# Optimization experiments

Measured on AMD Instinct MI355X. Metric: run time of the kernel, lower is better.

Reference implementation:

```python
import jax, jax.numpy as jnp
import numpy as np

N = 100000      # nodes
E = 1600000     # edges
F_IN = 512      # num_features
H = 128         # hidden
C = 40          # num_classes
K = 10          # Chebyshev order


def setup_inputs() -> dict:
    key = jax.random.key(0)
    ks = jax.random.split(key, 6)
    x = jax.random.normal(ks[0], (N, F_IN), dtype=jnp.float32)
    edge_index = jax.random.randint(ks[1], (2, E), 0, N, dtype=jnp.int32)
    W1 = jax.random.normal(ks[2], (F_IN, H), dtype=jnp.float32) / np.sqrt(F_IN).astype(np.float32)
    b1 = jnp.zeros((H,), dtype=jnp.float32)
    W2 = jax.random.normal(ks[3], (H, C), dtype=jnp.float32) / np.sqrt(H).astype(np.float32)
    b2 = jnp.zeros((C,), dtype=jnp.float32)
    # Chebyshev coefficients temp[K+1]
    temp = 1.0 + 0.1 * jax.random.normal(ks[4], (K + 1,), dtype=jnp.float32)
    return {"x": x, "edge_index": edge_index, "W1": W1, "b1": b1, "W2": W2, "b2": b2, "temp": temp}


def reference(x, edge_index, W1, b1, W2, b2, temp):
    # MLP encoder (eval mode: dropout is identity)
    h = jax.nn.relu(x @ W1 + b1)          # [N, H]
    h = h @ W2 + b2                        # [N, C]

    # gcn_norm: add self-loops, symmetric normalization
    self_loop = jnp.arange(N, dtype=edge_index.dtype)
    row = jnp.concatenate([edge_index[0], self_loop])   # [E+N]
    col = jnp.concatenate([edge_index[1], self_loop])
    deg = jax.ops.segment_sum(jnp.ones_like(row, dtype=jnp.float32), row, num_segments=N)
    dis = jnp.where(deg > 0, jax.lax.rsqrt(jnp.maximum(deg, 1.0)), 0.0)
    norm = dis[row] * dis[col]             # [E+N]

    def prop(v):  # A_hat @ v : gather-scale-scatter over edges
        return jax.ops.segment_sum(norm[:, None] * v[col], row, num_segments=N)

    # Chebyshev recurrence: Tx_k = 2*A_hat*Tx_{k-1} - Tx_{k-2}
    Tx0 = h
    Tx1 = prop(h)
    out0 = temp[0] * Tx0 + temp[1] * Tx1

    def body(carry, coe):
        t0, t1, acc = carry
        t2 = 2.0 * prop(t1) - t0
        return (t1, t2, acc + coe * t2), None

    (_, _, out), _ = jax.lax.scan(body, (Tx0, Tx1, out0), temp[2:])
    return jax.nn.log_softmax(out, axis=1)
```

## Files before the change

### kernel.cpp

```cpp
#include <hip/hip_runtime.h>
#include <hip/hip_bf16.h>
#include <cstdint>
#include <cstddef>

#define NN   100000
#define EE   1600000
#define FIN  512
#define HID  128
#define CC   40
#define KORD 10

typedef __attribute__((ext_vector_type(4))) float f4;
typedef __attribute__((ext_vector_type(8))) short short8_t;
typedef __attribute__((ext_vector_type(2))) unsigned int u2;

__device__ __forceinline__ unsigned short cvt_bf16(float f) {
  union { float f; unsigned u; } a; a.f = f;
  unsigned r = a.u + 0x7fffu + ((a.u >> 16) & 1u);
  return (unsigned short)(r >> 16);
}
__device__ __forceinline__ unsigned pk_bf(float a, float b) {
  union { float f; unsigned u; } x, y; x.f = a; y.f = b;
  unsigned ra = x.u + 0x7fffu + ((x.u >> 16) & 1u);
  unsigned rb = y.u + 0x7fffu + ((y.u >> 16) & 1u);
  return (ra >> 16) | (rb & 0xffff0000u);
}
__device__ __forceinline__ f4 cvf(u2 p) {
  union { unsigned u; float f; } a, b, c, d;
  a.u = p.x << 16; b.u = p.x & 0xffff0000u;
  c.u = p.y << 16; d.u = p.y & 0xffff0000u;
  f4 r; r.x = a.f; r.y = b.f; r.z = c.f; r.w = d.f; return r;
}

__global__ __launch_bounds__(256) void k_deg(const int* __restrict__ rowI, int* __restrict__ deg) {
  int i = blockIdx.x * 256 + threadIdx.x;
  if (i < EE) atomicAdd(&deg[rowI[i]], 1);
}

__global__ __launch_bounds__(256) void k_finalize(int* __restrict__ deg, float* __restrict__ dis,
                                                  float* __restrict__ sqd, float* __restrict__ invd) {
  int i = blockIdx.x * 256 + threadIdx.x;
  if (i < NN) {
    int d = deg[i] + 1;
    deg[i] = d;
    float fd = (float)d;
    dis[i]  = rsqrtf(fd);
    sqd[i]  = sqrtf(fd);
    invd[i] = 1.0f / fd;
  }
}

__global__ __launch_bounds__(256) void k_scan1(const int* __restrict__ cnt, int* __restrict__ excl,
                                               int* __restrict__ bsums) {
  __shared__ int s[256];
  int tid = threadIdx.x;
  int base = blockIdx.x * 1024 + tid * 4;
  int v0 = (base + 0 < NN) ? cnt[base + 0] : 0;
  int v1 = (base + 1 < NN) ? cnt[base + 1] : 0;
  int v2 = (base + 2 < NN) ? cnt[base + 2] : 0;
  int v3 = (base + 3 < NN) ? cnt[base + 3] : 0;
  int tsum = v0 + v1 + v2 + v3;
  s[tid] = tsum;
  __syncthreads();
  for (int off = 1; off < 256; off <<= 1) {
    int t = (tid >= off) ? s[tid - off] : 0;
    __syncthreads();
    if (tid >= off) s[tid] += t;
    __syncthreads();
  }
  int run = s[tid] - tsum;
  if (tid == 255) bsums[blockIdx.x] = s[255];
  if (base + 0 < NN) excl[base + 0] = run; run += v0;
  if (base + 1 < NN) excl[base + 1] = run; run += v1;
  if (base + 2 < NN) excl[base + 2] = run; run += v2;
  if (base + 3 < NN) excl[base + 3] = run;
}

__global__ __launch_bounds__(128) void k_scan2(int* __restrict__ bsums, int nb) {
  __shared__ int s[128];
  int tid = threadIdx.x;
  int v = (tid < nb) ? bsums[tid] : 0;
  s[tid] = v;
  __syncthreads();
  for (int off = 1; off < 128; off <<= 1) {
    int t = (tid >= off) ? s[tid - off] : 0;
    __syncthreads();
    if (tid >= off) s[tid] += t;
    __syncthreads();
  }
  if (tid < nb) bsums[tid] = s[tid] - v;
}

__global__ __launch_bounds__(256) void k_scan3(const int* __restrict__ cnt, int* __restrict__ rs,
                                               int* __restrict__ cur, const int* __restrict__ bsums) {
  int i = blockIdx.x * 256 + threadIdx.x;
  if (i < NN) {
    int v = rs[i] + bsums[i >> 10];
    rs[i] = v;
    cur[i] = v;
    if (i == NN - 1) rs[NN] = v + cnt[i];
  }
}

__global__ __launch_bounds__(256) void k_scatter(const int* __restrict__ rowI, const int* __restrict__ colI,
                                                 int* __restrict__ cur, int* __restrict__ colS) {
  int i = blockIdx.x * 256 + threadIdx.x;
  if (i >= EE + NN) return;
  int r, c;
  if (i < EE) { r = rowI[i]; c = colI[i]; }
  else        { r = i - EE;  c = r; }
  int pos = atomicAdd(&cur[r], 1);
  colS[pos] = c * 80;
}

__global__ __launch_bounds__(256) void k_w1t(const float* __restrict__ W1, unsigned short* __restrict__ W1T) {
  int idx = blockIdx.x * 256 + threadIdx.x;
  int k = idx >> 7;
  int n = idx & 127;
  float v = W1[idx];
  W1T[(k >> 5) * 4096 + n * 32 + (k & 31)] = cvt_bf16(v);
}

#define LDK 40
__global__ __launch_bounds__(256) void k_gemm1(const float* __restrict__ x, const unsigned short* __restrict__ W1T,
                                               const float* __restrict__ b1, float* __restrict__ h1) {
  __shared__ __align__(16) short As_s[128][LDK];
  __shared__ __align__(16) short Bs_s[128][LDK];
  int tid  = threadIdx.x;
  int wave = tid >> 6, lane = tid & 63;
  int blockRow = blockIdx.x * 128;
  int wr = (wave & 1) * 64, wc = (wave >> 1) * 64;
  int l15 = lane & 15, lk = (lane >> 4) * 8;

  int ar = tid >> 1, ak = (tid & 1) * 16;

  f4 acc[4][4] = {};

  for (int k0 = 0; k0 < FIN; k0 += 32) {
    int gr = blockRow + ar;
    f4 xv0 = {0.f,0.f,0.f,0.f}, xv1 = xv0, xv2 = xv0, xv3 = xv0;
    if (gr < NN) {
      const float* xr = x + (size_t)gr * FIN + k0 + ak;
      xv0 = *(const f4*)&xr[0];
      xv1 = *(const f4*)&xr[4];
      xv2 = *(const f4*)&xr[8];
      xv3 = *(const f4*)&xr[12];
    }
    short8_t p0, p1;
#pragma unroll
    for (int q = 0; q < 4; ++q) {
      p0[q]     = (short)cvt_bf16(xv0[q]);
      p0[q + 4] = (short)cvt_bf16(xv1[q]);
      p1[q]     = (short)cvt_bf16(xv2[q]);
      p1[q + 4] = (short)cvt_bf16(xv3[q]);
    }
    *(short8_t*)&As_s[ar][ak]     = p0;
    *(short8_t*)&As_s[ar][ak + 8] = p1;

    const unsigned short* Wt = W1T + (k0 >> 5) * 4096;
    short8_t q0 = *(const short8_t*)&Wt[tid * 16];
    short8_t q1 = *(const short8_t*)&Wt[tid * 16 + 8];
    int bn = tid >> 1, bkk = (tid & 1) * 16;
    *(short8_t*)&Bs_s[bn][bkk]     = q0;
    *(short8_t*)&Bs_s[bn][bkk + 8] = q1;

    __syncthreads();

    short8_t afr[4], bfr[4];
#pragma unroll
    for (int m = 0; m < 4; ++m) afr[m] = *(const short8_t*)&As_s[wr + m * 16 + l15][lk];
#pragma unroll
    for (int n = 0; n < 4; ++n) bfr[n] = *(const short8_t*)&Bs_s[wc + n * 16 + l15][lk];
#pragma unroll
    for (int m = 0; m < 4; ++m)
#pragma unroll
      for (int n = 0; n < 4; ++n)
        acc[m][n] = __builtin_amdgcn_mfma_f32_16x16x32_bf16(afr[m], bfr[n], acc[m][n], 0, 0, 0);

    __syncthreads();
  }

  float bias[4];
#pragma unroll
  for (int n = 0; n < 4; ++n) bias[n] = b1[wc + n * 16 + l15];
#pragma unroll
  for (int m = 0; m < 4; ++m) {
    int baseRow = blockRow + wr + m * 16 + (lane >> 4) * 4;
#pragma unroll
    for (int n = 0; n < 4; ++n) {
      int col = wc + n * 16 + l15;
#pragma unroll
      for (int r = 0; r < 4; ++r) {
        int grow = baseRow + r;
        if (grow < NN) h1[(size_t)grow * HID + col] = fmaxf(acc[m][n][r] + bias[n], 0.f);
      }
    }
  }
}

__global__ __launch_bounds__(256) void k_gemm2(const float* __restrict__ h1, const float* __restrict__ W2,
                                               const float* __restrict__ b2, const float* __restrict__ temp,
                                               const float* __restrict__ dis,
                                               float* __restrict__ w0, float* __restrict__ outAcc) {
  __shared__ float sW[HID * CC];
  __shared__ float sb[CC];
  int tid = threadIdx.x;
  for (int i = tid; i < HID * CC; i += 256) sW[i] = W2[i];
  if (tid < CC) sb[tid] = b2[tid];
  __syncthreads();
  int gid = blockIdx.x * 256 + tid;
  int row = gid / CC;
  int col = gid - row * CC;
  const float* hr = h1 + (size_t)row * HID;
  float acc = sb[col];
#pragma unroll 8
  for (int k = 0; k < HID; ++k) acc = fmaf(hr[k], sW[k * CC + col], acc);
  outAcc[gid] = temp[0] * acc;
  w0[gid] = acc * dis[row];
}

__global__ __launch_bounds__(256) void k_cvt(const float* __restrict__ v, unsigned short* __restrict__ sh) {
  int i = blockIdx.x * 256 + threadIdx.x;
  if (i * 4 >= NN * CC) return;
  f4 t = *(const f4*)&v[i * 4];
  u2 p; p.x = pk_bf(t.x, t.y); p.y = pk_bf(t.z, t.w);
  *(u2*)&sh[i * 4] = p;
}

template <int MODE>
__global__ __launch_bounds__(256) void k_prop(const unsigned short* __restrict__ shIn,
                                              unsigned short* __restrict__ shOut,
                                              float* __restrict__ vio,
                                              float* __restrict__ outAcc,
                                              const int* __restrict__ colS,
                                              const int* __restrict__ rs,
                                              const float* __restrict__ invd, const float* __restrict__ sqd,
                                              const float* __restrict__ temp, int kIdx) {
  int lane = threadIdx.x & 63;
  int wave = threadIdx.x >> 6;
  int sub  = lane / 10;
  int fi   = lane - sub * 10;
  int node = blockIdx.x * 24 + wave * 6 + sub;
  bool active = (sub < 6) && (node < NN);
  int s = 0, e = 0;
  if (active) { s = rs[node]; e = rs[node + 1]; }
  const char* base = (const char*)shIn + fi * 8;
  f4 a0 = {0.f,0.f,0.f,0.f}, a1 = a0, a2 = a0, a3 = a0;
  int j = s;
  for (; j + 8 <= e; j += 8) {
    int c0 = colS[j],     c1 = colS[j + 1], c2 = colS[j + 2], c3 = colS[j + 3];
    int c4 = colS[j + 4], c5 = colS[j + 5], c6 = colS[j + 6], c7 = colS[j + 7];
    u2 p0 = *(const u2*)(base + c0);
    u2 p1 = *(const u2*)(base + c1);
    u2 p2 = *(const u2*)(base + c2);
    u2 p3 = *(const u2*)(base + c3);
    u2 p4 = *(const u2*)(base + c4);
    u2 p5 = *(const u2*)(base + c5);
    u2 p6 = *(const u2*)(base + c6);
    u2 p7 = *(const u2*)(base + c7);
    a0 += cvf(p0); a1 += cvf(p1); a2 += cvf(p2); a3 += cvf(p3);
    a0 += cvf(p4); a1 += cvf(p5); a2 += cvf(p6); a3 += cvf(p7);
  }
  if (j + 4 <= e) {
    int c0 = colS[j], c1 = colS[j + 1], c2 = colS[j + 2], c3 = colS[j + 3];
    u2 p0 = *(const u2*)(base + c0);
    u2 p1 = *(const u2*)(base + c1);
    u2 p2 = *(const u2*)(base + c2);
    u2 p3 = *(const u2*)(base + c3);
    a0 += cvf(p0); a1 += cvf(p1); a2 += cvf(p2); a3 += cvf(p3);
    j += 4;
  }
  if (j + 2 <= e) {
    u2 p0 = *(const u2*)(base + colS[j]);
    u2 p1 = *(const u2*)(base + colS[j + 1]);
    a0 += cvf(p0); a1 += cvf(p1);
    j += 2;
  }
  if (j < e) a2 += cvf(*(const u2*)(base + colS[j]));

  if (active) {
    f4 sum = (a0 + a1) + (a2 + a3);
    float iv = invd[node], sq = sqd[node], tk = temp[kIdx];
    size_t o = (size_t)node * CC + fi * 4;
    f4 w;
    if (MODE == 0) w = iv * sum;
    else { f4 prev = *(const f4*)&vio[o]; w = (2.f * iv) * sum - prev; }
    *(f4*)&vio[o] = w;
    u2 p; p.x = pk_bf(w.x, w.y); p.y = pk_bf(w.z, w.w);
    *(u2*)((char*)shOut + (size_t)node * 80 + fi * 8) = p;
    f4 oa = *(const f4*)&outAcc[o];
    *(f4*)&outAcc[o] = oa + (tk * sq) * w;
  }
}

__global__ __launch_bounds__(256) void k_lsm(float* __restrict__ out) {
  int row = blockIdx.x * 256 + threadIdx.x;
  if (row >= NN) return;
  float* p = out + (size_t)row * CC;
  float v[CC];
#pragma unroll
  for (int i = 0; i < CC / 4; ++i) *(f4*)&v[i * 4] = *(const f4*)&p[i * 4];
  float m = v[0];
#pragma unroll
  for (int i = 1; i < CC; ++i) m = fmaxf(m, v[i]);
  float ssum = 0.f;
#pragma unroll
  for (int i = 0; i < CC; ++i) ssum += expf(v[i] - m);
  float lse = m + logf(ssum);
#pragma unroll
  for (int i = 0; i < CC; ++i) v[i] -= lse;
#pragma unroll
  for (int i = 0; i < CC / 4; ++i) *(f4*)&p[i * 4] = *(f4*)&v[i * 4];
}

extern "C" void kernel_launch(void* const* d_in, const int* in_sizes, int n_in,
                              void* d_out, int out_size, void* d_ws, size_t ws_size,
                              hipStream_t stream) {
  const float* x    = (const float*)d_in[0];
  const int*   ei   = (const int*)d_in[1];
  const float* W1   = (const float*)d_in[2];
  const float* b1   = (const float*)d_in[3];
  const float* W2   = (const float*)d_in[4];
  const float* b2   = (const float*)d_in[5];
  const float* temp = (const float*)d_in[6];
  const int* rowI = ei;
  const int* colI = ei + EE;
  float* out = (float*)d_out;

  char* w = (char*)d_ws;
  auto alloc = [&](size_t bytes) -> void* {
    void* p = (void*)w;
    w += (bytes + 255) & ~(size_t)255;
    return p;
  };
  float* t0    = (float*)alloc((size_t)NN * CC * 4);
  float* t1    = (float*)alloc((size_t)NN * CC * 4);
  int*   deg   = (int*)  alloc((size_t)NN * 4);
  float* dis   = (float*)alloc((size_t)NN * 4);
  float* sqd   = (float*)alloc((size_t)NN * 4);
  float* invd  = (float*)alloc((size_t)NN * 4);
  int*   rs    = (int*)  alloc((size_t)(NN + 1) * 4);
  int*   cur   = (int*)  alloc((size_t)NN * 4);
  int*   bsums = (int*)  alloc(512 * 4);
  unsigned short* W1T = (unsigned short*)alloc((size_t)FIN * HID * 2);
  char* big = (char*)alloc((size_t)NN * HID * 4);
  float* h1 = (float*)big;
  int*   colS = (int*)big;
  unsigned short* sh0 = (unsigned short*)(big + ((size_t)8 << 20));
  unsigned short* sh1 = (unsigned short*)(big + ((size_t)16 << 20));

  hipMemsetAsync(deg, 0, (size_t)NN * 4, stream);

  k_deg<<<(EE + 255) / 256, 256, 0, stream>>>(rowI, deg);
  k_finalize<<<(NN + 255) / 256, 256, 0, stream>>>(deg, dis, sqd, invd);

  int nb = (NN + 1023) / 1024;
  k_scan1<<<nb, 256, 0, stream>>>(deg, rs, bsums);
  k_scan2<<<1, 128, 0, stream>>>(bsums, nb);
  k_scan3<<<(NN + 255) / 256, 256, 0, stream>>>(deg, rs, cur, bsums);

  k_w1t<<<FIN * HID / 256, 256, 0, stream>>>(W1, W1T);
  k_gemm1<<<(NN + 127) / 128, 256, 0, stream>>>(x, W1T, b1, h1);
  k_gemm2<<<(NN * CC) / 256, 256, 0, stream>>>(h1, W2, b2, temp, dis, t0, out);

  k_scatter<<<(EE + NN + 255) / 256, 256, 0, stream>>>(rowI, colI, cur, colS);
  k_cvt<<<(NN * CC / 4 + 255) / 256, 256, 0, stream>>>(t0, sh0);

  int G = (NN + 23) / 24;
  unsigned short* sh[2] = {sh0, sh1};
  float* tb[2] = {t0, t1};
  k_prop<0><<<G, 256, 0, stream>>>(sh[0], sh[1], t1, out, colS, rs, invd, sqd, temp, 1);
  for (int k = 2; k <= KORD; ++k) {
    k_prop<1><<<G, 256, 0, stream>>>(sh[(k - 1) & 1], sh[k & 1], tb[k & 1], out, colS, rs, invd, sqd, temp, k);
  }

  k_lsm<<<(NN + 255) / 256, 256, 0, stream>>>(out);
}
```

Baseline: 745.5 us.

## Fuse setup kernels, degree-sort nodes, widen prop gathers to 16 bytes

Several small setup kernels are merged into combined launches: degree counting with the W1 transpose, scan2 with a histogram scan, scan3 with building a degree-sorted permutation, and the edge scatter with the GEMM1 launch. The scatter now runs alongside GEMM1 instead of after it, which requires colS to move to its own buffer rather than aliasing h1. The propagation kernel now assigns 5 lanes per node with 16-byte bf16 gathers, 12 nodes per wave, and processes nodes in degree-sorted order for better load balance. This reduces launch count and per-edge load instructions, at the cost of extra atomics and a permutation indirection that breaks sequential output writes.

```diff
diff --git a/kernel.cpp b/kernel.cpp
--- a/kernel.cpp
+++ b/kernel.cpp
@@ -12,7 +12,7 @@
 
 typedef __attribute__((ext_vector_type(4))) float f4;
 typedef __attribute__((ext_vector_type(8))) short short8_t;
-typedef __attribute__((ext_vector_type(2))) unsigned int u2;
+typedef __attribute__((ext_vector_type(4))) unsigned int u4;
 
 __device__ __forceinline__ unsigned short cvt_bf16(float f) {
   union { float f; unsigned u; } a; a.f = f;
@@ -25,20 +25,30 @@
   unsigned rb = y.u + 0x7fffu + ((y.u >> 16) & 1u);
   return (ra >> 16) | (rb & 0xffff0000u);
 }
-__device__ __forceinline__ f4 cvf(u2 p) {
+__device__ __forceinline__ f4 cvf2(unsigned lo, unsigned hi) {
   union { unsigned u; float f; } a, b, c, d;
-  a.u = p.x << 16; b.u = p.x & 0xffff0000u;
-  c.u = p.y << 16; d.u = p.y & 0xffff0000u;
+  a.u = lo << 16; b.u = lo & 0xffff0000u;
+  c.u = hi << 16; d.u = hi & 0xffff0000u;
   f4 r; r.x = a.f; r.y = b.f; r.z = c.f; r.w = d.f; return r;
 }
 
-__global__ __launch_bounds__(256) void k_deg(const int* __restrict__ rowI, int* __restrict__ deg) {
-  int i = blockIdx.x * 256 + threadIdx.x;
-  if (i < EE) atomicAdd(&deg[rowI[i]], 1);
+__global__ __launch_bounds__(256) void k_dw(const int* __restrict__ rowI, int* __restrict__ deg,
+                                            const float* __restrict__ W1, unsigned short* __restrict__ W1T,
+                                            int ndeg) {
+  int b = blockIdx.x;
+  if (b < ndeg) {
+    int i = b * 256 + threadIdx.x;
+    if (i < EE) atomicAdd(&deg[rowI[i]], 1);
+  } else {
+    int idx = (b - ndeg) * 256 + threadIdx.x;
+    int k = idx >> 7, n = idx & 127;
+    W1T[(k >> 5) * 4096 + n * 32 + (k & 31)] = cvt_bf16(W1[idx]);
+  }
 }
 
 __global__ __launch_bounds__(256) void k_finalize(int* __restrict__ deg, float* __restrict__ dis,
-                                                  float* __restrict__ sqd, float* __restrict__ invd) {
+                                                  float* __restrict__ sqd, float* __restrict__ invd,
+                                                  int* __restrict__ hist) {
   int i = blockIdx.x * 256 + threadIdx.x;
   if (i < NN) {
     int d = deg[i] + 1;
@@ -47,6 +57,7 @@
     dis[i]  = rsqrtf(fd);
     sqd[i]  = sqrtf(fd);
     invd[i] = 1.0f / fd;
+    atomicAdd(&hist[min(d, 255)], 1);
   }
 }
 
@@ -76,62 +87,85 @@
   if (base + 3 < NN) excl[base + 3] = run;
 }
 
-__global__ __launch_bounds__(128) void k_scan2(int* __restrict__ bsums, int nb) {
-  __shared__ int s[128];
+__global__ __launch_bounds__(256) void k_scan2h(int* __restrict__ bsums, int nb, int* __restrict__ hist) {
+  __shared__ int s[256];
   int tid = threadIdx.x;
-  int v = (tid < nb) ? bsums[tid] : 0;
-  s[tid] = v;
-  __syncthreads();
-  for (int off = 1; off < 128; off <<= 1) {
-    int t = (tid >= off) ? s[tid - off] : 0;
-    __syncthreads();
-    if (tid >= off) s[tid] += t;
-    __syncthreads();
-  }
-  if (tid < nb) bsums[tid] = s[tid] - v;
-}
-
-__global__ __launch_bounds__(256) void k_scan3(const int* __restrict__ cnt, int* __restrict__ rs,
-                                               int* __restrict__ cur, const int* __restrict__ bsums) {
-  int i = blockIdx.x * 256 + threadIdx.x;
-  if (i < NN) {
-    int v = rs[i] + bsums[i >> 10];
-    rs[i] = v;
-    cur[i] = v;
-    if (i == NN - 1) rs[NN] = v + cnt[i];
-  }
-}
-
-__global__ __launch_bounds__(256) void k_scatter(const int* __restrict__ rowI, const int* __restrict__ colI,
-                                                 int* __restrict__ cur, int* __restrict__ colS) {
-  int i = blockIdx.x * 256 + threadIdx.x;
-  if (i >= EE + NN) return;
-  int r, c;
-  if (i < EE) { r = rowI[i]; c = colI[i]; }
-  else        { r = i - EE;  c = r; }
-  int pos = atomicAdd(&cur[r], 1);
-  colS[pos] = c * 80;
-}
-
-__global__ __launch_bounds__(256) void k_w1t(const float* __restrict__ W1, unsigned short* __restrict__ W1T) {
-  int idx = blockIdx.x * 256 + threadIdx.x;
-  int k = idx >> 7;
-  int n = idx & 127;
-  float v = W1[idx];
-  W1T[(k >> 5) * 4096 + n * 32 + (k & 31)] = cvt_bf16(v);
+  if (blockIdx.x == 0) {
+    int v = (tid < nb) ? bsums[tid] : 0;
+    s[tid] = v;
+    __syncthreads();
+    for (int off = 1; off < 256; off <<= 1) {
+      int t = (tid >= off) ? s[tid - off] : 0;
+      __syncthreads();
+      if (tid >= off) s[tid] += t;
+      __syncthreads();
+    }
+    if (tid < nb) bsums[tid] = s[tid] - v;
+  } else {
+    int v = hist[tid];
+    s[tid] = v;
+    __syncthreads();
+    for (int off = 1; off < 256; off <<= 1) {
+      int t = (tid >= off) ? s[tid - off] : 0;
+      __syncthreads();
+      if (tid >= off) s[tid] += t;
+      __syncthreads();
+    }
+    hist[tid] = s[tid] - v;
+  }
+}
+
+__global__ __launch_bounds__(256) void k_scan3p(const int* __restrict__ cnt, int* __restrict__ rs,
+                                                int* __restrict__ cur, const int* __restrict__ bsums,
+                                                const int* __restrict__ hoff, int* __restrict__ hcnt,
+                                                int* __restrict__ perm, int nb3) {
+  int b = blockIdx.x;
+  int tid = threadIdx.x;
+  if (b < nb3) {
+    int i = b * 256 + tid;
+    if (i < NN) {
+      int v = rs[i] + bsums[i >> 10];
+      rs[i] = v;
+      cur[i] = v;
+      if (i == NN - 1) rs[NN] = v + cnt[i];
+    }
+  } else {
+    int i = (b - nb3) * 256 + tid;
+    if (i < NN) {
+      int d = min(cnt[i], 255);
+      int pos = hoff[d] + atomicAdd(&hcnt[d], 1);
+      perm[pos] = i;
+    }
+  }
 }
 
 #define LDK 40
-__global__ __launch_bounds__(256) void k_gemm1(const float* __restrict__ x, const unsigned short* __restrict__ W1T,
-                                               const float* __restrict__ b1, float* __restrict__ h1) {
+__global__ __launch_bounds__(256) void k_g1sc(const float* __restrict__ x, const unsigned short* __restrict__ W1T,
+                                              const float* __restrict__ b1, float* __restrict__ h1,
+                                              const int* __restrict__ rowI, const int* __restrict__ colI,
+                                              int* __restrict__ cur, int* __restrict__ colS, int ng1) {
   __shared__ __align__(16) short As_s[128][LDK];
   __shared__ __align__(16) short Bs_s[128][LDK];
+  if (blockIdx.x >= ng1) {
+    int bid = blockIdx.x - ng1;
+#pragma unroll
+    for (int t = 0; t < 4; ++t) {
+      int i = bid * 1024 + t * 256 + threadIdx.x;
+      if (i < EE + NN) {
+        int r, c;
+        if (i < EE) { r = rowI[i]; c = colI[i]; }
+        else        { r = i - EE;  c = r; }
+        int pos = atomicAdd(&cur[r], 1);
+        colS[pos] = c * 80;
+      }
+    }
+    return;
+  }
   int tid  = threadIdx.x;
   int wave = tid >> 6, lane = tid & 63;
   int blockRow = blockIdx.x * 128;
   int wr = (wave & 1) * 64, wc = (wave >> 1) * 64;
   int l15 = lane & 15, lk = (lane >> 4) * 8;
-
   int ar = tid >> 1, ak = (tid & 1) * 16;
 
   f4 acc[4][4] = {};
@@ -223,8 +257,9 @@
   int i = blockIdx.x * 256 + threadIdx.x;
   if (i * 4 >= NN * CC) return;
   f4 t = *(const f4*)&v[i * 4];
-  u2 p; p.x = pk_bf(t.x, t.y); p.y = pk_bf(t.z, t.w);
-  *(u2*)&sh[i * 4] = p;
+  unsigned lo = pk_bf(t.x, t.y), hi = pk_bf(t.z, t.w);
+  unsigned long long p = (unsigned long long)lo | ((unsigned long long)hi << 32);
+  *(unsigned long long*)&sh[i * 4] = p;
 }
 
 template <int MODE>
@@ -234,62 +269,69 @@
                                               float* __restrict__ outAcc,
                                               const int* __restrict__ colS,
                                               const int* __restrict__ rs,
+                                              const int* __restrict__ perm,
                                               const float* __restrict__ invd, const float* __restrict__ sqd,
                                               const float* __restrict__ temp, int kIdx) {
   int lane = threadIdx.x & 63;
   int wave = threadIdx.x >> 6;
-  int sub  = lane / 10;
-  int fi   = lane - sub * 10;
-  int node = blockIdx.x * 24 + wave * 6 + sub;
-  bool active = (sub < 6) && (node < NN);
-  int s = 0, e = 0;
-  if (active) { s = rs[node]; e = rs[node + 1]; }
-  const char* base = (const char*)shIn + fi * 8;
-  f4 a0 = {0.f,0.f,0.f,0.f}, a1 = a0, a2 = a0, a3 = a0;
+  int grp  = lane / 5;
+  int fi   = lane - grp * 5;
+  int nidx = blockIdx.x * 48 + wave * 12 + grp;
+  bool active = (grp < 12) && (nidx < NN);
+  int node = 0, s = 0, e = 0;
+  if (active) { node = perm[nidx]; s = rs[node]; e = rs[node + 1]; }
+  const char* base = (const char*)shIn + fi * 16;
+  f4 lo0 = {0.f,0.f,0.f,0.f}, hi0 = lo0, lo1 = lo0, hi1 = lo0;
+  f4 lo2 = lo0, hi2 = lo0, lo3 = lo0, hi3 = lo0;
   int j = s;
-  for (; j + 8 <= e; j += 8) {
-    int c0 = colS[j],     c1 = colS[j + 1], c2 = colS[j + 2], c3 = colS[j + 3];
-    int c4 = colS[j + 4], c5 = colS[j + 5], c6 = colS[j + 6], c7 = colS[j + 7];
-    u2 p0 = *(const u2*)(base + c0);
-    u2 p1 = *(const u2*)(base + c1);
-    u2 p2 = *(const u2*)(base + c2);
-    u2 p3 = *(const u2*)(base + c3);
-    u2 p4 = *(const u2*)(base + c4);
-    u2 p5 = *(const u2*)(base + c5);
-    u2 p6 = *(const u2*)(base + c6);
-    u2 p7 = *(const u2*)(base + c7);
-    a0 += cvf(p0); a1 += cvf(p1); a2 += cvf(p2); a3 += cvf(p3);
-    a0 += cvf(p4); a1 += cvf(p5); a2 += cvf(p6); a3 += cvf(p7);
-  }
-  if (j + 4 <= e) {
+  for (; j + 4 <= e; j += 4) {
     int c0 = colS[j], c1 = colS[j + 1], c2 = colS[j + 2], c3 = colS[j + 3];
-    u2 p0 = *(const u2*)(base + c0);
-    u2 p1 = *(const u2*)(base + c1);
-    u2 p2 = *(const u2*)(base + c2);
-    u2 p3 = *(const u2*)(base + c3);
-    a0 += cvf(p0); a1 += cvf(p1); a2 += cvf(p2); a3 += cvf(p3);
-    j += 4;
+    u4 p0 = *(const u4*)(base + c0);
+    u4 p1 = *(const u4*)(base + c1);
+    u4 p2 = *(const u4*)(base + c2);
+    u4 p3 = *(const u4*)(base + c3);
+    lo0 += cvf2(p0.x, p0.y); hi0 += cvf2(p0.z, p0.w);
+    lo1 += cvf2(p1.x, p1.y); hi1 += cvf2(p1.z, p1.w);
+    lo2 += cvf2(p2.x, p2.y); hi2 += cvf2(p2.z, p2.w);
+    lo3 += cvf2(p3.x, p3.y); hi3 += cvf2(p3.z, p3.w);
   }
   if (j + 2 <= e) {
-    u2 p0 = *(const u2*)(base + colS[j]);
-    u2 p1 = *(const u2*)(base + colS[j + 1]);
-    a0 += cvf(p0); a1 += cvf(p1);
+    int c0 = colS[j], c1 = colS[j + 1];
+    u4 p0 = *(const u4*)(base + c0);
+    u4 p1 = *(const u4*)(base + c1);
+    lo0 += cvf2(p0.x, p0.y); hi0 += cvf2(p0.z, p0.w);
+    lo1 += cvf2(p1.x, p1.y); hi1 += cvf2(p1.z, p1.w);
     j += 2;
   }
-  if (j < e) a2 += cvf(*(const u2*)(base + colS[j]));
+  if (j < e) {
+    u4 p0 = *(const u4*)(base + colS[j]);
+    lo2 += cvf2(p0.x, p0.y); hi2 += cvf2(p0.z, p0.w);
+  }
 
   if (active) {
-    f4 sum = (a0 + a1) + (a2 + a3);
+    f4 slo = (lo0 + lo1) + (lo2 + lo3);
+    f4 shi = (hi0 + hi1) + (hi2 + hi3);
     float iv = invd[node], sq = sqd[node], tk = temp[kIdx];
-    size_t o = (size_t)node * CC + fi * 4;
-    f4 w;
-    if (MODE == 0) w = iv * sum;
-    else { f4 prev = *(const f4*)&vio[o]; w = (2.f * iv) * sum - prev; }
-    *(f4*)&vio[o] = w;
-    u2 p; p.x = pk_bf(w.x, w.y); p.y = pk_bf(w.z, w.w);
-    *(u2*)((char*)shOut + (size_t)node * 80 + fi * 8) = p;
-    f4 oa = *(const f4*)&outAcc[o];
-    *(f4*)&outAcc[o] = oa + (tk * sq) * w;
+    size_t o = (size_t)node * CC + fi * 8;
+    f4 wlo, whi;
+    if (MODE == 0) { wlo = iv * slo; whi = iv * shi; }
+    else {
+      f4 plo = *(const f4*)&vio[o];
+      f4 phi = *(const f4*)&vio[o + 4];
+      wlo = (2.f * iv) * slo - plo;
+      whi = (2.f * iv) * shi - phi;
+    }
+    *(f4*)&vio[o]     = wlo;
+    *(f4*)&vio[o + 4] = whi;
+    u4 pk;
+    pk.x = pk_bf(wlo.x, wlo.y); pk.y = pk_bf(wlo.z, wlo.w);
+    pk.z = pk_bf(whi.x, whi.y); pk.w = pk_bf(whi.z, whi.w);
+    *(u4*)((char*)shOut + (size_t)node * 80 + fi * 16) = pk;
+    f4 olo = *(const f4*)&outAcc[o];
+    f4 ohi = *(const f4*)&outAcc[o + 4];
+    float ts = tk * sq;
+    *(f4*)&outAcc[o]     = olo + ts * wlo;
+    *(f4*)&outAcc[o + 4] = ohi + ts * whi;
   }
 }
 
@@ -341,37 +383,47 @@
   float* invd  = (float*)alloc((size_t)NN * 4);
   int*   rs    = (int*)  alloc((size_t)(NN + 1) * 4);
   int*   cur   = (int*)  alloc((size_t)NN * 4);
+  int*   perm  = (int*)  alloc((size_t)NN * 4);
   int*   bsums = (int*)  alloc(512 * 4);
+  int*   hist  = (int*)  alloc(256 * 4);
+  int*   hcnt  = (int*)  alloc(256 * 4);
   unsigned short* W1T = (unsigned short*)alloc((size_t)FIN * HID * 2);
+  int*   colS  = (int*)  alloc((size_t)(EE + NN) * 4);
   char* big = (char*)alloc((size_t)NN * HID * 4);
   float* h1 = (float*)big;
-  int*   colS = (int*)big;
-  unsigned short* sh0 = (unsigned short*)(big + ((size_t)8 << 20));
-  unsigned short* sh1 = (unsigned short*)(big + ((size_t)16 << 20));
+  unsigned short* sh0 = (unsigned short*)big;
+  unsigned short* sh1 = (unsigned short*)(big + ((size_t)8 << 20));
 
   hipMemsetAsync(deg, 0, (size_t)NN * 4, stream);
-
-  k_deg<<<(EE + 255) / 256, 256, 0, stream>>>(rowI, deg);
-  k_finalize<<<(NN + 255) / 256, 256, 0, stream>>>(deg, dis, sqd, invd);
+  hipMemsetAsync(hist, 0, 256 * 4, stream);
+  hipMemsetAsync(hcnt, 0, 256 * 4, stream);
+
+  const int NDEG = (EE + 255) / 256;
+  const int NW1T = FIN * HID / 256;
+  k_dw<<<NDEG + NW1T, 256, 0, stream>>>(rowI, deg, W1, W1T, NDEG);
+
+  k_finalize<<<(NN + 255) / 256, 256, 0, stream>>>(deg, dis, sqd, invd, hist);
 
   int nb = (NN + 1023) / 1024;
   k_scan1<<<nb, 256, 0, stream>>>(deg, rs, bsums);
-  k_scan2<<<1, 128, 0, stream>>>(bsums, nb);
-  k_scan3<<<(NN + 255) / 256, 256, 0, stream>>>(deg, rs, cur, bsums);
-
-  k_w1t<<<FIN * HID / 256, 256, 0, stream>>>(W1, W1T);
-  k_gemm1<<<(NN + 127) / 128, 256, 0, stream>>>(x, W1T, b1, h1);
+  k_scan2h<<<2, 256, 0, stream>>>(bsums, nb, hist);
+  int nb3 = (NN + 255) / 256;
+  k_scan3p<<<2 * nb3, 256, 0, stream>>>(deg, rs, cur, bsums, hist, hcnt, perm, nb3);
+
+  const int NG1 = (NN + 127) / 128;
+  const int NSC = (EE + NN + 1023) / 1024;
+  k_g1sc<<<NG1 + NSC, 256, 0, stream>>>(x, W1T, b1, h1, rowI, colI, cur, colS, NG1);
+
   k_gemm2<<<(NN * CC) / 256, 256, 0, stream>>>(h1, W2, b2, temp, dis, t0, out);
 
-  k_scatter<<<(EE + NN + 255) / 256, 256, 0, stream>>>(rowI, colI, cur, colS);
   k_cvt<<<(NN * CC / 4 + 255) / 256, 256, 0, stream>>>(t0, sh0);
 
-  int G = (NN + 23) / 24;
+  int G = (NN + 47) / 48;
   unsigned short* sh[2] = {sh0, sh1};
   float* tb[2] = {t0, t1};
-  k_prop<0><<<G, 256, 0, stream>>>(sh[0], sh[1], t1, out, colS, rs, invd, sqd, temp, 1);
+  k_prop<0><<<G, 256, 0, stream>>>(sh[0], sh[1], t1, out, colS, rs, perm, invd, sqd, temp, 1);
   for (int k = 2; k <= KORD; ++k) {
-    k_prop<1><<<G, 256, 0, stream>>>(sh[(k - 1) & 1], sh[k & 1], tb[k & 1], out, colS, rs, invd, sqd, temp, k);
+    k_prop<1><<<G, 256, 0, stream>>>(sh[(k - 1) & 1], sh[k & 1], tb[k & 1], out, colS, rs, perm, invd, sqd, temp, k);
   }
 
   k_lsm<<<(NN + 255) / 256, 256, 0, stream>>>(out);
```

Result: slower. 1.402 ms (+88.1%).
